# Optimization experiments

Measured on AMD Instinct MI355X. Metric: run time of the kernel, lower is better.

The kernel has to match this reference:

```python
import jax, jax.numpy as jnp
import numpy as np

T = 4096; D = 768; V = 32000; L = 4; EPS = 1e-5


def _ln(x, g, b):
    m = jnp.mean(x, axis=-1, keepdims=True)
    v = jnp.mean((x - m) ** 2, axis=-1, keepdims=True)
    return (x - m) * jax.lax.rsqrt(v + EPS) * g + b


def _qgelu(x):
    return x * jax.nn.sigmoid(1.702 * x)


def setup_inputs() -> dict:
    key = jax.random.key(0)
    ks = jax.random.split(key, 10)
    s = 0.02
    return {
        "idx": jax.random.randint(ks[0], (T,), 0, V),
        "wte": jax.random.normal(ks[1], (V, D)) * s,
        "rb_ln_g": jnp.ones((D,)), "rb_ln_b": jnp.zeros((D,)),
        "rb_fc_w": jax.random.normal(ks[2], (D, 4 * D)) * s,
        "rb_fc_b": jnp.zeros((4 * D,)),
        "rb_proj_w": jax.random.normal(ks[3], (4 * D, D)) * s,
        "rb_proj_b": jnp.zeros((D,)),
        "lnf_g": jnp.ones((D,)), "lnf_b": jnp.zeros((D,)),
        "lm_head_w": jax.random.normal(ks[4], (D, V)) * s,
        "mb_ln_g": jnp.ones((L, 2 * D)), "mb_ln_b": jnp.zeros((L, 2 * D)),
        "mb_fc_w": jax.random.normal(ks[5], (L, 2 * D, 4 * D)) * s,
        "mb_fc_b": jnp.zeros((L, 4 * D)),
        "mb_proj_w": jax.random.normal(ks[6], (L, 4 * D, D)) * s,
        "mb_proj_b": jnp.zeros((L, D)),
        "op_w": jax.random.normal(ks[7], (L, D, D)) * s,
        "op_b": jnp.zeros((L, D)),
        "lns_g": jnp.ones((L, D)), "lns_b": jnp.zeros((L, D)),
        "heads_w": jax.random.normal(ks[8], (L, D, V)) * s,
    }


def reference(idx, wte, rb_ln_g, rb_ln_b, rb_fc_w, rb_fc_b, rb_proj_w, rb_proj_b,
              lnf_g, lnf_b, lm_head_w, mb_ln_g, mb_ln_b, mb_fc_w, mb_fc_b,
              mb_proj_w, mb_proj_b, op_w, op_b, lns_g, lns_b, heads_w):
    # token embedding (dropout is identity in eval) + initial residual block
    x = wte[idx]  # [T, D]
    h = _ln(x, rb_ln_g, rb_ln_b)
    x = x + _qgelu(h @ rb_fc_w + rb_fc_b) @ rb_proj_w + rb_proj_b
    x = _ln(x, lnf_g, lnf_b)
    logits = x @ lm_head_w  # [T, V]

    # targets=None path: pred_targets = cat(idx[1:], [-1])
    pred_targets = jnp.concatenate([idx[1:], jnp.full((1,), -1, idx.dtype)])
    pos = jnp.arange(T)
    skey = jax.random.key(42)

    for i in range(L):  # static small loop over layers
        j = i + 1
        # multinomial(softmax(logits), 1) == categorical(logits)
        idx_next = jax.random.categorical(jax.random.fold_in(skey, i), logits)
        # positions p where the sample matched the next-token target and p < T - j
        mask = (idx_next == pred_targets) & (pos < T - j)  # [T] bool
        # x2[p] = x[p + j] (padded); compute merge densely, select with mask
        x2 = jnp.concatenate([x[j:], jnp.zeros((j, D), x.dtype)], axis=0)
        h = _ln(jnp.concatenate([x, x2], axis=-1), mb_ln_g[i], mb_ln_b[i])
        merged = x2 + _qgelu(h @ mb_fc_w[i] + mb_fc_b[i]) @ mb_proj_w[i] + mb_proj_b[i]
        # scatter merged[p] into x at position p + j where mask[p]
        merged_s = jnp.concatenate([jnp.zeros((j, D), x.dtype), merged[:-j]], axis=0)
        mask_s = jnp.concatenate([jnp.zeros((j,), bool), mask[:-j]], axis=0)
        x = jnp.where(mask_s[:, None], merged_s, x)
        x = x @ op_w[i] + op_b[i]
        x = _ln(x, lns_g[i], lns_b[i])
        logits = x @ heads_w[i]
    return logits
```

## Files before the change

### kernel.cpp

```cpp
#include <hip/hip_runtime.h>
#include <cstdint>
#include <cstddef>

#define T_TOK 4096
#define DIM   768
#define VOCAB 32000
#define NLAYER 4
#define HALF_TV 65536000u

typedef short bf16x8 __attribute__((ext_vector_type(8)));
typedef float f32x4  __attribute__((ext_vector_type(4)));
typedef float f32x4v __attribute__((ext_vector_type(4)));

__host__ __device__ inline void tf2x32(uint32_t k0, uint32_t k1, uint32_t& v0, uint32_t& v1){
  uint32_t ks2 = k0 ^ k1 ^ 0x1BD11BDAu;
  uint32_t x0 = v0 + k0, x1 = v1 + k1;
#define TFR(R) { x0 += x1; x1 = (x1<<R)|(x1>>(32-R)); x1 ^= x0; }
  TFR(13) TFR(15) TFR(26) TFR(6)
  x0 += k1;  x1 += ks2 + 1u;
  TFR(17) TFR(29) TFR(16) TFR(24)
  x0 += ks2; x1 += k0 + 2u;
  TFR(13) TFR(15) TFR(26) TFR(6)
  x0 += k0;  x1 += k1 + 3u;
  TFR(17) TFR(29) TFR(16) TFR(24)
  x0 += k1;  x1 += ks2 + 4u;
  TFR(13) TFR(15) TFR(26) TFR(6)
  x0 += ks2; x1 += k0 + 5u;
#undef TFR
  v0 = x0; v1 = x1;
}

__device__ inline float neglog_u(uint32_t k){
  float L;
  if (k >= 0x780000u){
    float x = (float)(0x800000u - k) * 1.1920928955078125e-7f;
    L = x * fmaf(x, fmaf(x, fmaf(x, 0.25f, 0.3333333333333f), 0.5f), 1.0f);
  } else {
    float l2k = __builtin_amdgcn_logf((float)k);
    L = 0.69314718055994531f * (23.0f - l2k);
    if (k == 0u) L = 87.33654475055310898f;
  }
  return L;
}

__device__ inline void gumbel_pair(uint32_t kf0, uint32_t kf1, uint32_t t_up, uint32_t v,
                                   float& gu, float& gd){
  uint32_t m = t_up * (uint32_t)VOCAB + v;
  uint32_t x0 = m, x1 = m + HALF_TV;
  tf2x32(kf0, kf1, x0, x1);
  float Lu = neglog_u(x0 >> 9);
  float Ld = neglog_u(x1 >> 9);
  gu = -0.69314718055994531f * __builtin_amdgcn_logf(Lu);
  gd = -0.69314718055994531f * __builtin_amdgcn_logf(Ld);
}

__device__ inline unsigned short f2bf(float f){
  uint32_t u = __float_as_uint(f);
  return (unsigned short)((u + 0x7FFFu + ((u >> 16) & 1u)) >> 16);
}
__device__ inline float bf2f(unsigned short h){
  return __uint_as_float(((uint32_t)h) << 16);
}
__device__ inline void cvt8(const float* f, bool lo, unsigned short* out){
  #pragma unroll
  for (int e=0;e<8;e++){
    float x = f[e];
    unsigned short h = f2bf(x);
    if (lo) h = f2bf(x - bf2f(h));
    out[e] = h;
  }
}
__device__ inline float blockReduceSum(float v){
  __shared__ float red[4];
  #pragma unroll
  for (int off=32; off>0; off>>=1) v += __shfl_down(v, off);
  int w = threadIdx.x >> 6;
  __syncthreads();
  if ((threadIdx.x & 63) == 0) red[w] = v;
  __syncthreads();
  return red[0] + red[1] + red[2] + red[3];
}

__device__ inline void gload16(const void* g, void* l){
  __builtin_amdgcn_global_load_lds(
      (const __attribute__((address_space(1))) unsigned int*)g,
      (__attribute__((address_space(3))) unsigned int*)l, 16, 0, 0);
}

enum { ST_F32 = 0, ST_HILO = 1, ST_SAMPLE = 2 };

template<int KSTEPS, int NSEG, bool BIAS, bool QGELU, bool RES, int STORE, bool NTST>
__global__ __launch_bounds__(256) void k_hgemm(
    const unsigned short* __restrict__ A0, const unsigned short* __restrict__ A1,
    const unsigned short* __restrict__ B0, const unsigned short* __restrict__ B2,
    float* __restrict__ C, unsigned short* __restrict__ Ch, unsigned short* __restrict__ Cl,
    const float* __restrict__ bias, const float* __restrict__ res,
    int N, uint32_t kf0, uint32_t kf1, unsigned long long* __restrict__ row_best)
{
  constexpr int K = KSTEPS * 64;
  __shared__ unsigned short sA[128*64];
  __shared__ unsigned short sB[128*64];
  const int t = threadIdx.x;
  const int wave = t >> 6, lane = t & 63;
  const int wm = wave >> 1, wn = wave & 1;
  const int g = lane >> 4, r = lane & 15;
  const int lr = lane >> 3, lc = lane & 7;

  int bid = blockIdx.x;
  int xcd = bid & 7, c = bid >> 3;
  int bm = xcd*4 + (c & 3);
  int bn = c >> 2;

  f32x4 acc[4][4] = {};

  for (int kb = 0; kb < NSEG*KSTEPS; ++kb){
    const int seg = (NSEG == 1) ? 0 : (kb / KSTEPS);
    const int k0  = (NSEG == 1) ? kb*64 : (kb % KSTEPS) * 64;
    const unsigned short* Ap = (seg == 1) ? A1 : A0;
    const unsigned short* Bp = (seg == 2) ? B2 : B0;
    __syncthreads();
    #pragma unroll
    for (int p=0;p<4;p++){
      int mr = p*32 + wave*8 + lr;
      int blk = mr >> 4;
      int grow = bm*64 + ((blk>>1)<<4) + (mr & 15) + ((blk & 1) ? 2048 : 0);
      int gk = k0 + ((lc ^ lr) << 3);
      gload16(Ap + (size_t)grow * K + gk, (char*)sA + mr*128 + lc*16);
      int nrow = bn*128 + mr;
      gload16(Bp + (size_t)nrow * K + gk, (char*)sB + mr*128 + lc*16);
    }
    __syncthreads();
    #pragma unroll
    for (int kk=0;kk<2;kk++){
      bf16x8 av[4], bv[4];
      #pragma unroll
      for (int mi=0;mi<4;mi++){
        int tr = wm*64 + mi*16 + r;
        av[mi] = *(const bf16x8*)((const char*)sA + tr*128 + (((kk*4+g) ^ (r&7))<<4));
      }
      #pragma unroll
      for (int ni=0;ni<4;ni++){
        int tr = wn*64 + ni*16 + r;
        bv[ni] = *(const bf16x8*)((const char*)sB + tr*128 + (((kk*4+g) ^ (r&7))<<4));
      }
      if constexpr (STORE == ST_SAMPLE) __builtin_amdgcn_s_setprio(1);
      #pragma unroll
      for (int mi=0;mi<4;mi++)
        #pragma unroll
        for (int ni=0;ni<4;ni++)
          acc[mi][ni] = __builtin_amdgcn_mfma_f32_16x16x32_bf16(av[mi], bv[ni], acc[mi][ni], 0, 0, 0);
      if constexpr (STORE == ST_SAMPLE) __builtin_amdgcn_s_setprio(0);
    }
  }

  if constexpr (STORE == ST_SAMPLE){
    #pragma unroll
    for (int mi=0; mi<4; mi+=2){
      int row16 = ((wm*4 + mi) >> 1) << 4;
      #pragma unroll
      for (int jj=0;jj<4;jj++){
        uint32_t t_up = bm*64 + row16 + g*4 + jj;
        unsigned long long bu = 0ull, bd = 0ull;
        #pragma unroll
        for (int ni=0;ni<4;ni++){
          uint32_t v = bn*128 + wn*64 + ni*16 + r;
          float gu, gd;
          gumbel_pair(kf0, kf1, t_up, v, gu, gd);
          float vu = acc[mi][ni][jj]   + gu;
          float vd = acc[mi+1][ni][jj] + gd;
          uint32_t fu = __float_as_uint(vu); fu = (fu & 0x80000000u) ? ~fu : (fu | 0x80000000u);
          uint32_t fd = __float_as_uint(vd); fd = (fd & 0x80000000u) ? ~fd : (fd | 0x80000000u);
          unsigned long long pu = ((unsigned long long)fu << 32) | (unsigned long long)(~v);
          unsigned long long pd = ((unsigned long long)fd << 32) | (unsigned long long)(~v);
          if (pu > bu) bu = pu;
          if (pd > bd) bd = pd;
        }
        #pragma unroll
        for (int off=1; off<16; off<<=1){
          unsigned int l0 = (unsigned int)bu, h0 = (unsigned int)(bu>>32);
          unsigned int l1 = __shfl_xor(l0, off), h1 = __shfl_xor(h0, off);
          unsigned long long o = ((unsigned long long)h1 << 32) | (unsigned long long)l1;
          if (o > bu) bu = o;
          l0 = (unsigned int)bd; h0 = (unsigned int)(bd>>32);
          l1 = __shfl_xor(l0, off); h1 = __shfl_xor(h0, off);
          o = ((unsigned long long)h1 << 32) | (unsigned long long)l1;
          if (o > bd) bd = o;
        }
        if (r == 0){
          atomicMax(&row_best[t_up], bu);
          atomicMax(&row_best[t_up + 2048], bd);
        }
      }
    }
  } else {
    #pragma unroll
    for (int mi=0;mi<4;mi++){
      int blk2 = wm*4 + mi;
      int mbase = bm*64 + ((blk2>>1)<<4) + ((blk2 & 1) ? 2048 : 0);
      #pragma unroll
      for (int ni=0;ni<4;ni++){
        int n = bn*128 + wn*64 + ni*16 + r;
        float bv_ = BIAS ? bias[n] : 0.0f;
        #pragma unroll
        for (int jj=0;jj<4;jj++){
          int m = mbase + g*4 + jj;
          float v = acc[mi][ni][jj] + bv_;
          if constexpr (QGELU) v = v / (1.0f + expf(-1.702f * v));
          if constexpr (RES)   v += res[(size_t)m * N + n];
          if constexpr (STORE == ST_F32){
            if constexpr (NTST) __builtin_nontemporal_store(v, &C[(size_t)m * N + n]);
            else                C[(size_t)m * N + n] = v;
          } else {
            unsigned short h = f2bf(v);
            Ch[(size_t)m * N + n] = h;
            Cl[(size_t)m * N + n] = f2bf(v - bf2f(h));
          }
        }
      }
    }
  }
}

template<bool SPLIT>
__global__ __launch_bounds__(256) void k_wt_t(const float* __restrict__ W,
    unsigned short* __restrict__ Bh, unsigned short* __restrict__ Bl, int K, int N)
{
  __shared__ unsigned short sH[64][72];
  __shared__ unsigned short sL[64][72];
  int kt = blockIdx.x, nt = blockIdx.y;
  int t = threadIdx.x;
  int kr = t >> 4, nc4 = (t & 15) * 4;
  #pragma unroll
  for (int p=0;p<4;p++){
    int k = p*16 + kr;
    f32x4v w = __builtin_nontemporal_load((const f32x4v*)&W[(size_t)(kt*64 + k) * N + nt*64 + nc4]);
    #pragma unroll
    for (int e=0;e<4;e++){
      unsigned short h = f2bf(w[e]);
      sH[nc4+e][k] = h;
      if (SPLIT) sL[nc4+e][k] = f2bf(w[e] - bf2f(h));
    }
  }
  __syncthreads();
  #pragma unroll
  for (int q=0;q<2;q++){
    int cid = t + q*256;
    int n = cid >> 3, ch = cid & 7;
    *(bf16x8*)&Bh[(size_t)(nt*64+n)*K + kt*64 + ch*8] = *(const bf16x8*)&sH[n][ch*8];
    if (SPLIT)
      *(bf16x8*)&Bl[(size_t)(nt*64+n)*K + kt*64 + ch*8] = *(const bf16x8*)&sL[n][ch*8];
  }
}

__global__ __launch_bounds__(256) void k_embed_ln(const int* __restrict__ idx,
    const float* __restrict__ wte, const float* __restrict__ g, const float* __restrict__ b,
    float* __restrict__ Xraw, unsigned short* __restrict__ Hh, unsigned short* __restrict__ Hl)
{
  int row = blockIdx.x;
  const float* src = wte + (size_t)idx[row] * DIM;
  float v[3];
  #pragma unroll
  for (int jj=0;jj<3;jj++) v[jj] = src[threadIdx.x + jj*256];
  float s = blockReduceSum(v[0]+v[1]+v[2]);
  float mean = s * (1.0f/DIM);
  float s2 = 0;
  #pragma unroll
  for (int jj=0;jj<3;jj++){ float d = v[jj]-mean; s2 += d*d; }
  s2 = blockReduceSum(s2);
  float rs = rsqrtf(s2 * (1.0f/DIM) + 1e-5f);
  #pragma unroll
  for (int jj=0;jj<3;jj++){
    int d = threadIdx.x + jj*256;
    Xraw[(size_t)row*DIM + d] = v[jj];
    float o = (v[jj]-mean)*rs*g[d] + b[d];
    unsigned short h = f2bf(o);
    Hh[(size_t)row*DIM + d] = h;
    Hl[(size_t)row*DIM + d] = f2bf(o - bf2f(h));
  }
}

__global__ __launch_bounds__(256) void k_ln(const float* __restrict__ in, float* __restrict__ out,
    const float* __restrict__ g, const float* __restrict__ b,
    unsigned short* __restrict__ obf, unsigned short* __restrict__ olo)
{
  int row = blockIdx.x;
  const float* src = in + (size_t)row * DIM;
  float v[3];
  #pragma unroll
  for (int jj=0;jj<3;jj++) v[jj] = src[threadIdx.x + jj*256];
  float s = blockReduceSum(v[0]+v[1]+v[2]);
  float mean = s * (1.0f/DIM);
  float s2 = 0;
  #pragma unroll
  for (int jj=0;jj<3;jj++){ float d = v[jj]-mean; s2 += d*d; }
  s2 = blockReduceSum(s2);
  float rs = rsqrtf(s2 * (1.0f/DIM) + 1e-5f);
  #pragma unroll
  for (int jj=0;jj<3;jj++){
    int d = threadIdx.x + jj*256;
    float o = (v[jj]-mean)*rs*g[d] + b[d];
    out[(size_t)row*DIM + d] = o;
    unsigned short h = f2bf(o);
    obf[(size_t)row*DIM + d] = h;
    olo[(size_t)row*DIM + d] = f2bf(o - bf2f(h));
  }
}

__global__ void k_mask(const unsigned long long* __restrict__ row_best,
    const int* __restrict__ idx, int j, int* __restrict__ count, int* __restrict__ plist)
{
  int t = blockIdx.x * blockDim.x + threadIdx.x;
  if (t >= T_TOK) return;
  int v = (int)(~(uint32_t)(row_best[t] & 0xFFFFFFFFull));
  int tgt = (t < T_TOK-1) ? idx[t+1] : -1;
  if (v == tgt && t < T_TOK - j){
    int pos = atomicAdd(count, 1);
    plist[pos] = t;
  }
}

__global__ __launch_bounds__(256) void k_merge(const float* __restrict__ X,
    const int* __restrict__ plist, const int* __restrict__ count,
    const float* __restrict__ lng, const float* __restrict__ lnb,
    const float* __restrict__ fcw, const float* __restrict__ fcb,
    const float* __restrict__ pjw, const float* __restrict__ pjb,
    float* __restrict__ mergebuf, int j)
{
  __shared__ float sh[1536 + 3072];
  int nb = *count;
  for (int bIdx = blockIdx.x; bIdx < nb; bIdx += gridDim.x){
    int p = plist[bIdx];
    const float* xp = X + (size_t)p * DIM;
    const float* x2 = X + (size_t)(p + j) * DIM;
    for (int d = threadIdx.x; d < 1536; d += 256)
      sh[d] = (d < DIM) ? xp[d] : x2[d - DIM];
    __syncthreads();
    float s = 0;
    for (int d = threadIdx.x; d < 1536; d += 256) s += sh[d];
    s = blockReduceSum(s);
    float mean = s * (1.0f/1536.0f);
    float s2 = 0;
    for (int d = threadIdx.x; d < 1536; d += 256){ float df = sh[d]-mean; s2 += df*df; }
    s2 = blockReduceSum(s2);
    float rs = rsqrtf(s2 * (1.0f/1536.0f) + 1e-5f);
    __syncthreads();
    for (int d = threadIdx.x; d < 1536; d += 256)
      sh[d] = (sh[d]-mean)*rs*lng[d] + lnb[d];
    __syncthreads();
    float* act = sh + 1536;
    #pragma unroll
    for (int jj=0;jj<12;jj++){
      int n = threadIdx.x + jj*256;
      float a = fcb[n];
      for (int k=0;k<1536;k++) a += sh[k]*fcw[(size_t)k*3072 + n];
      act[n] = a / (1.0f + expf(-1.702f*a));
    }
    __syncthreads();
    #pragma unroll
    for (int jj=0;jj<3;jj++){
      int d = threadIdx.x + jj*256;
      float a = pjb[d];
      for (int k=0;k<3072;k++) a += act[k]*pjw[(size_t)k*DIM + d];
      mergebuf[(size_t)bIdx*DIM + d] = x2[d] + a;
    }
    __syncthreads();
  }
}

__global__ void k_scatter(float* __restrict__ X, unsigned short* __restrict__ Xbf,
    unsigned short* __restrict__ Xlo, const float* __restrict__ mergebuf,
    const int* __restrict__ plist, const int* __restrict__ count, int j)
{
  int nb = *count;
  for (int bIdx = blockIdx.x; bIdx < nb; bIdx += gridDim.x){
    int p = plist[bIdx];
    for (int d = threadIdx.x; d < DIM; d += 256){
      float v = mergebuf[(size_t)bIdx*DIM + d];
      size_t o = (size_t)(p + j)*DIM + d;
      X[o] = v;
      unsigned short h = f2bf(v);
      Xbf[o] = h;
      Xlo[o] = f2bf(v - bf2f(h));
    }
  }
}

__global__ __launch_bounds__(256) void k_gemm_old(
    const float* __restrict__ A, const float* __restrict__ B, float* __restrict__ C,
    int M, int N, int K)
{
  __shared__ unsigned short sA[128*64];
  __shared__ unsigned short sB[128*64];
  const int t = threadIdx.x;
  const int bn = blockIdx.x, bm = blockIdx.y;
  const int wave = t >> 6, lane = t & 63;
  const int wm = wave >> 1, wn = wave & 1;
  const int g = lane >> 4, r = lane & 15;
  f32x4 acc[4][4] = {};
  const int nK = K >> 6;
  const int aC = t & 7,  aM0 = t >> 3;
  const int bN0 = t & 31, bC = t >> 5;
  const float* Abase = A + (size_t)(bm*128) * K;
  const float* Bbase = B + (size_t)(bn*128);
  for (int seg = 0; seg < 3; ++seg) {
    const bool aLO = (seg == 1), bLO = (seg == 2);
    for (int kb = 0; kb < nK; ++kb) {
      const int k0 = kb << 6;
      __syncthreads();
      #pragma unroll
      for (int p=0;p<4;p++){
        int m = p*32 + aM0;
        const float* src = Abase + (size_t)m * K + k0 + aC*8;
        float ff[8];
        *(float4*)(ff)   = *(const float4*)(src);
        *(float4*)(ff+4) = *(const float4*)(src+4);
        unsigned short hh[8];
        cvt8(ff, aLO, hh);
        *(bf16x8*)&sA[m*64 + ((aC ^ (m & 7)) * 8)] = *(bf16x8*)hh;
      }
      #pragma unroll
      for (int p=0;p<4;p++){
        int n = p*32 + bN0;
        float ff[8];
        const float* src = Bbase + (size_t)(k0 + bC*8) * N + n;
        #pragma unroll
        for (int e=0;e<8;e++) ff[e] = src[(size_t)e * N];
        unsigned short hh[8];
        cvt8(ff, bLO, hh);
        *(bf16x8*)&sB[n*64 + ((bC ^ (n & 7)) * 8)] = *(bf16x8*)hh;
      }
      __syncthreads();
      #pragma unroll
      for (int kk=0;kk<2;kk++){
        bf16x8 av[4], bv[4];
        #pragma unroll
        for (int mi=0;mi<4;mi++){
          int m = wm*64 + mi*16 + r;
          av[mi] = *(const bf16x8*)&sA[m*64 + (((kk*4 + g) ^ (m & 7)) * 8)];
        }
        #pragma unroll
        for (int ni=0;ni<4;ni++){
          int n = wn*64 + ni*16 + r;
          bv[ni] = *(const bf16x8*)&sB[n*64 + (((kk*4 + g) ^ (n & 7)) * 8)];
        }
        #pragma unroll
        for (int mi=0;mi<4;mi++)
          #pragma unroll
          for (int ni=0;ni<4;ni++)
            acc[mi][ni] = __builtin_amdgcn_mfma_f32_16x16x32_bf16(av[mi], bv[ni], acc[mi][ni], 0, 0, 0);
      }
    }
  }
  #pragma unroll
  for (int mi=0;mi<4;mi++)
    #pragma unroll
    for (int ni=0;ni<4;ni++)
      #pragma unroll
      for (int jj=0;jj<4;jj++){
        int m = bm*128 + wm*64 + mi*16 + g*4 + jj;
        int n = bn*128 + wn*64 + ni*16 + r;
        C[(size_t)m * N + n] = acc[mi][ni][jj];
      }
}

static void fold_key(uint32_t i, uint32_t& o0, uint32_t& o1){
  uint32_t x0 = 0, x1 = i;
  tf2x32(0u, 42u, x0, x1);
  o0 = x0; o1 = x1;
}

extern "C" void kernel_launch(void* const* d_in, const int* in_sizes, int n_in,
                              void* d_out, int out_size, void* d_ws, size_t ws_size,
                              hipStream_t stream)
{
  const int*   idx       = (const int*)  d_in[0];
  const float* wte       = (const float*)d_in[1];
  const float* rb_ln_g   = (const float*)d_in[2];
  const float* rb_ln_b   = (const float*)d_in[3];
  const float* rb_fc_w   = (const float*)d_in[4];
  const float* rb_fc_b   = (const float*)d_in[5];
  const float* rb_proj_w = (const float*)d_in[6];
  const float* rb_proj_b = (const float*)d_in[7];
  const float* lnf_g     = (const float*)d_in[8];
  const float* lnf_b     = (const float*)d_in[9];
  const float* lm_head_w = (const float*)d_in[10];
  const float* mb_ln_g   = (const float*)d_in[11];
  const float* mb_ln_b   = (const float*)d_in[12];
  const float* mb_fc_w   = (const float*)d_in[13];
  const float* mb_fc_b   = (const float*)d_in[14];
  const float* mb_proj_w = (const float*)d_in[15];
  const float* mb_proj_b = (const float*)d_in[16];
  const float* op_w      = (const float*)d_in[17];
  const float* op_b      = (const float*)d_in[18];
  const float* lns_g     = (const float*)d_in[19];
  const float* lns_b     = (const float*)d_in[20];
  const float* heads_w   = (const float*)d_in[21];

  const size_t TD = (size_t)T_TOK * DIM;
  const size_t DV = (size_t)DIM * VOCAB;

  float* X = (float*)d_ws;
  float* Y = X + TD;
  unsigned short* Xbf = (unsigned short*)(Y + TD);
  unsigned short* Xlo = Xbf + TD;
  unsigned short* BtFh = Xlo + TD;
  unsigned short* BtFl = BtFh + DV;
  size_t need_big = (size_t)((char*)(BtFl + DV) - (char*)d_ws);
  bool big = ws_size >= need_big;

  char* ob = (char*)d_out;
  float* OUT = (float*)d_out;
  unsigned short* Hh     = (unsigned short*)(ob);
  unsigned short* Hl     = Hh + TD;
  unsigned short* ACTh   = (unsigned short*)(ob + ((size_t)16<<20));
  unsigned short* ACTl   = ACTh + TD*4;
  unsigned short* Btfc_h = (unsigned short*)(ob + ((size_t)72<<20));
  unsigned short* Btfc_l = Btfc_h + (size_t)3072*DIM;
  unsigned short* Btpj_h = (unsigned short*)(ob + ((size_t)84<<20));
  unsigned short* Btpj_l = Btpj_h + (size_t)3072*DIM;
  unsigned short* BtS    = (unsigned short*)(ob + ((size_t)96<<20));
  unsigned short* Btop_h = (unsigned short*)(ob + ((size_t)152<<20));
  unsigned short* Btop_l = Btop_h + (size_t)DIM*DIM;
  float* MERGE = (float*)(ob + ((size_t)160<<20));
  unsigned long long* ROWBEST = (unsigned long long*)(ob + ((size_t)176<<20));
  int* PLIST = (int*)(ROWBEST + T_TOK);
  int* COUNT = PLIST + T_TOK;

  dim3 blk(256);

  k_embed_ln<<<T_TOK, blk, 0, stream>>>(idx, wte, rb_ln_g, rb_ln_b, X, Hh, Hl);
  k_wt_t<true><<<dim3(12,48), blk, 0, stream>>>(rb_fc_w,   Btfc_h, Btfc_l, DIM,  3072);
  k_wt_t<true><<<dim3(48,12), blk, 0, stream>>>(rb_proj_w, Btpj_h, Btpj_l, 3072, DIM);
  k_hgemm<12,3,true,true,false,ST_HILO,false><<<24*32, blk, 0, stream>>>(
      Hh, Hl, Btfc_h, Btfc_l, nullptr, ACTh, ACTl, rb_fc_b, nullptr, 3072, 0u,0u, nullptr);
  k_hgemm<48,3,true,false,true,ST_F32,false><<<6*32, blk, 0, stream>>>(
      ACTh, ACTl, Btpj_h, Btpj_l, Y, nullptr, nullptr, rb_proj_b, X, DIM, 0u,0u, nullptr);
  k_ln<<<T_TOK, blk, 0, stream>>>(Y, X, lnf_g, lnf_b, Xbf, Xlo);

  for (int i = 0; i < NLAYER; ++i){
    int j = i + 1;
    uint32_t kf0, kf1; fold_key((uint32_t)i, kf0, kf1);

    hipMemsetAsync(ROWBEST, 0, (size_t)T_TOK*8, stream);
    hipMemsetAsync(COUNT, 0, 4, stream);

    const float* hw = (i == 0) ? lm_head_w : heads_w + (size_t)(i-1)*DV;
    k_wt_t<false><<<dim3(12,500), blk, 0, stream>>>(hw, BtS, nullptr, DIM, VOCAB);
    k_hgemm<12,1,false,false,false,ST_SAMPLE,false><<<250*32, blk, 0, stream>>>(
        Xbf, Xbf, BtS, BtS, nullptr, nullptr, nullptr, nullptr, nullptr,
        VOCAB, kf0, kf1, ROWBEST);

    k_mask<<<T_TOK/256, blk, 0, stream>>>(ROWBEST, idx, j, COUNT, PLIST);
    k_merge<<<64, blk, 0, stream>>>(X, PLIST, COUNT,
        mb_ln_g + (size_t)i*1536, mb_ln_b + (size_t)i*1536,
        mb_fc_w + (size_t)i*1536*3072, mb_fc_b + (size_t)i*3072,
        mb_proj_w + (size_t)i*3072*DIM, mb_proj_b + (size_t)i*DIM, MERGE, j);
    k_scatter<<<64, blk, 0, stream>>>(X, Xbf, Xlo, MERGE, PLIST, COUNT, j);

    k_wt_t<true><<<dim3(12,12), blk, 0, stream>>>(op_w + (size_t)i*DIM*DIM, Btop_h, Btop_l, DIM, DIM);
    k_hgemm<12,3,true,false,false,ST_F32,false><<<6*32, blk, 0, stream>>>(
        Xbf, Xlo, Btop_h, Btop_l, Y, nullptr, nullptr, op_b + (size_t)i*DIM, nullptr,
        DIM, 0u,0u, nullptr);
    k_ln<<<T_TOK, blk, 0, stream>>>(Y, X, lns_g + (size_t)i*DIM, lns_b + (size_t)i*DIM, Xbf, Xlo);
  }

  if (big){
    k_wt_t<true><<<dim3(12,500), blk, 0, stream>>>(heads_w + (size_t)3*DV, BtFh, BtFl, DIM, VOCAB);
    k_hgemm<12,3,false,false,false,ST_F32,true><<<250*32, blk, 0, stream>>>(
        Xbf, Xlo, BtFh, BtFl, OUT, nullptr, nullptr, nullptr, nullptr, VOCAB, 0u,0u, nullptr);
  } else {
    k_gemm_old<<<dim3(VOCAB/128, T_TOK/128), blk, 0, stream>>>(
        X, heads_w + (size_t)3*DV, OUT, T_TOK, VOCAB, DIM);
  }
}
```

Measured before the change: 2.817 ms.

## Add 512-thread triple-buffered GEMM for vocab-sized sampling and final head

Adds a new GEMM kernel with 8 waves and 256x128 tiles for the large vocabulary GEMMs (sampling and the final logits). It uses a three-stage LDS ring with async global-to-LDS loads and explicit vmcnt waits, so loads for later k-tiles overlap MFMA work. This hides memory latency and halves the grid size. In exchange it uses about 144KB of LDS per block, which limits occupancy to one block per CU, and relies on hand-counted waitcnt values.

```diff
diff --git a/kernel.cpp b/kernel.cpp
--- a/kernel.cpp
+++ b/kernel.cpp
@@ -87,79 +87,112 @@
       (__attribute__((address_space(3))) unsigned int*)l, 16, 0, 0);
 }
 
+#define ASM_FENCE() asm volatile("" ::: "memory")
+
 enum { ST_F32 = 0, ST_HILO = 1, ST_SAMPLE = 2 };
 
-template<int KSTEPS, int NSEG, bool BIAS, bool QGELU, bool RES, int STORE, bool NTST>
-__global__ __launch_bounds__(256) void k_hgemm(
+template<int KSTEPS, int NSEG, int STORE, bool NTST>
+__global__ __launch_bounds__(512) void k_hgemm8(
     const unsigned short* __restrict__ A0, const unsigned short* __restrict__ A1,
     const unsigned short* __restrict__ B0, const unsigned short* __restrict__ B2,
-    float* __restrict__ C, unsigned short* __restrict__ Ch, unsigned short* __restrict__ Cl,
-    const float* __restrict__ bias, const float* __restrict__ res,
-    int N, uint32_t kf0, uint32_t kf1, unsigned long long* __restrict__ row_best)
-{
-  constexpr int K = KSTEPS * 64;
-  __shared__ unsigned short sA[128*64];
-  __shared__ unsigned short sB[128*64];
+    float* __restrict__ C, uint32_t kf0, uint32_t kf1,
+    unsigned long long* __restrict__ row_best, int N)
+{
+  constexpr int K  = KSTEPS * 64;
+  constexpr int NT = NSEG * KSTEPS;
+  __shared__ unsigned short sAll[3 * 24 * 1024];
+
   const int t = threadIdx.x;
-  const int wave = t >> 6, lane = t & 63;
-  const int wm = wave >> 1, wn = wave & 1;
-  const int g = lane >> 4, r = lane & 15;
-  const int lr = lane >> 3, lc = lane & 7;
+  const int w = t >> 6, l = t & 63;
+  const int wm = w >> 1, wn = w & 1;
+  const int g = l >> 4, r = l & 15;
+  const int lr = l >> 3, lc = l & 7;
 
   int bid = blockIdx.x;
   int xcd = bid & 7, c = bid >> 3;
-  int bm = xcd*4 + (c & 3);
-  int bn = c >> 2;
+  int bm = xcd*2 + (c & 1);
+  int bn = c >> 1;
 
   f32x4 acc[4][4] = {};
 
-  for (int kb = 0; kb < NSEG*KSTEPS; ++kb){
-    const int seg = (NSEG == 1) ? 0 : (kb / KSTEPS);
-    const int k0  = (NSEG == 1) ? kb*64 : (kb % KSTEPS) * 64;
+  size_t arow[4];
+  #pragma unroll
+  for (int p=0;p<4;p++){
+    int mr = p*64 + w*8 + lr;
+    int blk = mr >> 4;
+    int grow = bm*128 + ((blk>>1)<<4) + (mr & 15) + ((blk & 1) ? 2048 : 0);
+    arow[p] = (size_t)grow * K;
+  }
+  size_t brow[2];
+  #pragma unroll
+  for (int p=0;p<2;p++){
+    int nr = p*64 + w*8 + lr;
+    brow[p] = (size_t)(bn*128 + nr) * K;
+  }
+  const int swz = (lc ^ lr) << 3;
+  const int ldst = (w*8)*128 + l*16;
+
+  auto stage = [&](int vt){
+    int s = vt % 3;
+    int seg = (NSEG == 1) ? 0 : (vt / KSTEPS);
+    int k0  = ((NSEG == 1) ? vt : (vt % KSTEPS)) * 64;
     const unsigned short* Ap = (seg == 1) ? A1 : A0;
     const unsigned short* Bp = (seg == 2) ? B2 : B0;
-    __syncthreads();
-    #pragma unroll
-    for (int p=0;p<4;p++){
-      int mr = p*32 + wave*8 + lr;
-      int blk = mr >> 4;
-      int grow = bm*64 + ((blk>>1)<<4) + (mr & 15) + ((blk & 1) ? 2048 : 0);
-      int gk = k0 + ((lc ^ lr) << 3);
-      gload16(Ap + (size_t)grow * K + gk, (char*)sA + mr*128 + lc*16);
-      int nrow = bn*128 + mr;
-      gload16(Bp + (size_t)nrow * K + gk, (char*)sB + mr*128 + lc*16);
-    }
-    __syncthreads();
+    char* base = (char*)sAll + s * 49152;
+    #pragma unroll
+    for (int p=0;p<4;p++)
+      gload16(Ap + arow[p] + k0 + swz, base + p*8192 + ldst);
+    char* baseB = base + 32768;
+    #pragma unroll
+    for (int p=0;p<2;p++)
+      gload16(Bp + brow[p] + k0 + swz, baseB + p*8192 + ldst);
+  };
+
+  stage(0);
+  stage(1);
+  asm volatile("s_waitcnt vmcnt(6)" ::: "memory");
+  ASM_FENCE(); __builtin_amdgcn_s_barrier(); ASM_FENCE();
+
+  for (int vt = 0; vt < NT; ++vt){
+    if (vt + 2 < NT) stage(vt + 2);
+    if (vt + 2 < NT)      { asm volatile("s_waitcnt vmcnt(12)" ::: "memory"); }
+    else if (vt + 1 < NT) { asm volatile("s_waitcnt vmcnt(6)"  ::: "memory"); }
+    else                  { asm volatile("s_waitcnt vmcnt(0)"  ::: "memory"); }
+    ASM_FENCE(); __builtin_amdgcn_s_barrier(); ASM_FENCE();
+
+    const char* sA = (const char*)sAll + (vt % 3) * 49152;
+    const char* sB = sA + 32768;
     #pragma unroll
     for (int kk=0;kk<2;kk++){
       bf16x8 av[4], bv[4];
       #pragma unroll
       for (int mi=0;mi<4;mi++){
         int tr = wm*64 + mi*16 + r;
-        av[mi] = *(const bf16x8*)((const char*)sA + tr*128 + (((kk*4+g) ^ (r&7))<<4));
+        av[mi] = *(const bf16x8*)(sA + tr*128 + (((kk*4+g) ^ (r&7))<<4));
       }
       #pragma unroll
       for (int ni=0;ni<4;ni++){
         int tr = wn*64 + ni*16 + r;
-        bv[ni] = *(const bf16x8*)((const char*)sB + tr*128 + (((kk*4+g) ^ (r&7))<<4));
-      }
-      if constexpr (STORE == ST_SAMPLE) __builtin_amdgcn_s_setprio(1);
+        bv[ni] = *(const bf16x8*)(sB + tr*128 + (((kk*4+g) ^ (r&7))<<4));
+      }
+      __builtin_amdgcn_s_setprio(1);
       #pragma unroll
       for (int mi=0;mi<4;mi++)
         #pragma unroll
         for (int ni=0;ni<4;ni++)
           acc[mi][ni] = __builtin_amdgcn_mfma_f32_16x16x32_bf16(av[mi], bv[ni], acc[mi][ni], 0, 0, 0);
-      if constexpr (STORE == ST_SAMPLE) __builtin_amdgcn_s_setprio(0);
-    }
+      __builtin_amdgcn_s_setprio(0);
+    }
+    ASM_FENCE(); __builtin_amdgcn_s_barrier(); ASM_FENCE();
   }
 
   if constexpr (STORE == ST_SAMPLE){
     #pragma unroll
     for (int mi=0; mi<4; mi+=2){
-      int row16 = ((wm*4 + mi) >> 1) << 4;
+      int row16 = (wm*2 + (mi>>1)) * 16;
       #pragma unroll
       for (int jj=0;jj<4;jj++){
-        uint32_t t_up = bm*64 + row16 + g*4 + jj;
+        uint32_t t_up = bm*128 + row16 + g*4 + jj;
         unsigned long long bu = 0ull, bd = 0ull;
         #pragma unroll
         for (int ni=0;ni<4;ni++){
@@ -196,25 +229,104 @@
     #pragma unroll
     for (int mi=0;mi<4;mi++){
       int blk2 = wm*4 + mi;
-      int mbase = bm*64 + ((blk2>>1)<<4) + ((blk2 & 1) ? 2048 : 0);
+      int mbase = bm*128 + ((blk2>>1)<<4) + ((blk2 & 1) ? 2048 : 0);
       #pragma unroll
       for (int ni=0;ni<4;ni++){
         int n = bn*128 + wn*64 + ni*16 + r;
-        float bv_ = BIAS ? bias[n] : 0.0f;
         #pragma unroll
         for (int jj=0;jj<4;jj++){
           int m = mbase + g*4 + jj;
-          float v = acc[mi][ni][jj] + bv_;
-          if constexpr (QGELU) v = v / (1.0f + expf(-1.702f * v));
-          if constexpr (RES)   v += res[(size_t)m * N + n];
-          if constexpr (STORE == ST_F32){
-            if constexpr (NTST) __builtin_nontemporal_store(v, &C[(size_t)m * N + n]);
-            else                C[(size_t)m * N + n] = v;
-          } else {
-            unsigned short h = f2bf(v);
-            Ch[(size_t)m * N + n] = h;
-            Cl[(size_t)m * N + n] = f2bf(v - bf2f(h));
-          }
+          float v = acc[mi][ni][jj];
+          if constexpr (NTST) __builtin_nontemporal_store(v, &C[(size_t)m * N + n]);
+          else                C[(size_t)m * N + n] = v;
+        }
+      }
+    }
+  }
+}
+
+template<int KSTEPS, int NSEG, bool BIAS, bool QGELU, bool RES, int STORE>
+__global__ __launch_bounds__(256) void k_hgemm(
+    const unsigned short* __restrict__ A0, const unsigned short* __restrict__ A1,
+    const unsigned short* __restrict__ B0, const unsigned short* __restrict__ B2,
+    float* __restrict__ C, unsigned short* __restrict__ Ch, unsigned short* __restrict__ Cl,
+    const float* __restrict__ bias, const float* __restrict__ res,
+    int N, uint32_t kf0, uint32_t kf1, unsigned long long* __restrict__ row_best)
+{
+  constexpr int K = KSTEPS * 64;
+  __shared__ unsigned short sA[128*64];
+  __shared__ unsigned short sB[128*64];
+  const int t = threadIdx.x;
+  const int wave = t >> 6, lane = t & 63;
+  const int wm = wave >> 1, wn = wave & 1;
+  const int g = lane >> 4, r = lane & 15;
+  const int lr = lane >> 3, lc = lane & 7;
+
+  int bid = blockIdx.x;
+  int xcd = bid & 7, c = bid >> 3;
+  int bm = xcd*4 + (c & 3);
+  int bn = c >> 2;
+
+  f32x4 acc[4][4] = {};
+
+  for (int kb = 0; kb < NSEG*KSTEPS; ++kb){
+    const int seg = (NSEG == 1) ? 0 : (kb / KSTEPS);
+    const int k0  = (NSEG == 1) ? kb*64 : (kb % KSTEPS) * 64;
+    const unsigned short* Ap = (seg == 1) ? A1 : A0;
+    const unsigned short* Bp = (seg == 2) ? B2 : B0;
+    __syncthreads();
+    #pragma unroll
+    for (int p=0;p<4;p++){
+      int mr = p*32 + wave*8 + lr;
+      int blk = mr >> 4;
+      int grow = bm*64 + ((blk>>1)<<4) + (mr & 15) + ((blk & 1) ? 2048 : 0);
+      int gk = k0 + ((lc ^ lr) << 3);
+      gload16(Ap + (size_t)grow * K + gk, (char*)sA + mr*128 + lc*16);
+      int nrow = bn*128 + mr;
+      gload16(Bp + (size_t)nrow * K + gk, (char*)sB + mr*128 + lc*16);
+    }
+    __syncthreads();
+    #pragma unroll
+    for (int kk=0;kk<2;kk++){
+      bf16x8 av[4], bv[4];
+      #pragma unroll
+      for (int mi=0;mi<4;mi++){
+        int tr = wm*64 + mi*16 + r;
+        av[mi] = *(const bf16x8*)((const char*)sA + tr*128 + (((kk*4+g) ^ (r&7))<<4));
+      }
+      #pragma unroll
+      for (int ni=0;ni<4;ni++){
+        int tr = wn*64 + ni*16 + r;
+        bv[ni] = *(const bf16x8*)((const char*)sB + tr*128 + (((kk*4+g) ^ (r&7))<<4));
+      }
+      #pragma unroll
+      for (int mi=0;mi<4;mi++)
+        #pragma unroll
+        for (int ni=0;ni<4;ni++)
+          acc[mi][ni] = __builtin_amdgcn_mfma_f32_16x16x32_bf16(av[mi], bv[ni], acc[mi][ni], 0, 0, 0);
+    }
+  }
+
+  #pragma unroll
+  for (int mi=0;mi<4;mi++){
+    int blk2 = wm*4 + mi;
+    int mbase = bm*64 + ((blk2>>1)<<4) + ((blk2 & 1) ? 2048 : 0);
+    #pragma unroll
+    for (int ni=0;ni<4;ni++){
+      int n = bn*128 + wn*64 + ni*16 + r;
+      float bv_ = BIAS ? bias[n] : 0.0f;
+      #pragma unroll
+      for (int jj=0;jj<4;jj++){
+        int m = mbase + g*4 + jj;
+        float v = acc[mi][ni][jj] + bv_;
+        if constexpr (QGELU) v = v / (1.0f + expf(-1.702f * v));
+        if constexpr (RES)   v += res[(size_t)m * N + n];
+        if constexpr (STORE == ST_F32){
+          C[(size_t)m * N + n] = v;
+        } else {
+          unsigned short h = f2bf(v);
+          Ch[(size_t)m * N + n] = h;
+          Cl[(size_t)m * N + n] = f2bf(v - bf2f(h));
         }
       }
     }
@@ -527,13 +639,14 @@
   int* COUNT = PLIST + T_TOK;
 
   dim3 blk(256);
+  dim3 blk8(512);
 
   k_embed_ln<<<T_TOK, blk, 0, stream>>>(idx, wte, rb_ln_g, rb_ln_b, X, Hh, Hl);
   k_wt_t<true><<<dim3(12,48), blk, 0, stream>>>(rb_fc_w,   Btfc_h, Btfc_l, DIM,  3072);
   k_wt_t<true><<<dim3(48,12), blk, 0, stream>>>(rb_proj_w, Btpj_h, Btpj_l, 3072, DIM);
-  k_hgemm<12,3,true,true,false,ST_HILO,false><<<24*32, blk, 0, stream>>>(
+  k_hgemm<12,3,true,true,false,ST_HILO><<<24*32, blk, 0, stream>>>(
       Hh, Hl, Btfc_h, Btfc_l, nullptr, ACTh, ACTl, rb_fc_b, nullptr, 3072, 0u,0u, nullptr);
-  k_hgemm<48,3,true,false,true,ST_F32,false><<<6*32, blk, 0, stream>>>(
+  k_hgemm<48,3,true,false,true,ST_F32><<<6*32, blk, 0, stream>>>(
       ACTh, ACTl, Btpj_h, Btpj_l, Y, nullptr, nullptr, rb_proj_b, X, DIM, 0u,0u, nullptr);
   k_ln<<<T_TOK, blk, 0, stream>>>(Y, X, lnf_g, lnf_b, Xbf, Xlo);
 
@@ -546,9 +659,8 @@
 
     const float* hw = (i == 0) ? lm_head_w : heads_w + (size_t)(i-1)*DV;
     k_wt_t<false><<<dim3(12,500), blk, 0, stream>>>(hw, BtS, nullptr, DIM, VOCAB);
-    k_hgemm<12,1,false,false,false,ST_SAMPLE,false><<<250*32, blk, 0, stream>>>(
-        Xbf, Xbf, BtS, BtS, nullptr, nullptr, nullptr, nullptr, nullptr,
-        VOCAB, kf0, kf1, ROWBEST);
+    k_hgemm8<12,1,ST_SAMPLE,false><<<4000, blk8, 0, stream>>>(
+        Xbf, Xbf, BtS, BtS, nullptr, kf0, kf1, ROWBEST, VOCAB);
 
     k_mask<<<T_TOK/256, blk, 0, stream>>>(ROWBEST, idx, j, COUNT, PLIST);
     k_merge<<<64, blk, 0, stream>>>(X, PLIST, COUNT,
@@ -558,7 +670,7 @@
     k_scatter<<<64, blk, 0, stream>>>(X, Xbf, Xlo, MERGE, PLIST, COUNT, j);
 
     k_wt_t<true><<<dim3(12,12), blk, 0, stream>>>(op_w + (size_t)i*DIM*DIM, Btop_h, Btop_l, DIM, DIM);
-    k_hgemm<12,3,true,false,false,ST_F32,false><<<6*32, blk, 0, stream>>>(
+    k_hgemm<12,3,true,false,false,ST_F32><<<6*32, blk, 0, stream>>>(
         Xbf, Xlo, Btop_h, Btop_l, Y, nullptr, nullptr, op_b + (size_t)i*DIM, nullptr,
         DIM, 0u,0u, nullptr);
     k_ln<<<T_TOK, blk, 0, stream>>>(Y, X, lns_g + (size_t)i*DIM, lns_b + (size_t)i*DIM, Xbf, Xlo);
@@ -566,8 +678,8 @@
 
   if (big){
     k_wt_t<true><<<dim3(12,500), blk, 0, stream>>>(heads_w + (size_t)3*DV, BtFh, BtFl, DIM, VOCAB);
-    k_hgemm<12,3,false,false,false,ST_F32,true><<<250*32, blk, 0, stream>>>(
-        Xbf, Xlo, BtFh, BtFl, OUT, nullptr, nullptr, nullptr, nullptr, VOCAB, 0u,0u, nullptr);
+    k_hgemm8<12,3,ST_F32,true><<<4000, blk8, 0, stream>>>(
+        Xbf, Xlo, BtFh, BtFl, OUT, 0u, 0u, nullptr, VOCAB);
   } else {
     k_gemm_old<<<dim3(VOCAB/128, T_TOK/128), blk, 0, stream>>>(
         X, heads_w + (size_t)3*DV, OUT, T_TOK, VOCAB, DIM);
```

Result: slower. 3.114 ms (+10.6%).
